# Kernel optimization log

Hardware: AMD Instinct MI355X
Metric: run time of the kernel (lower is better)

## Reference

```python
import jax, jax.numpy as jnp
import numpy as np

N = 1_000_000   # pose-graph nodes
E = 2_000_000   # edges (odometry + loop closures)
M = N - 1
L1, L2, L3, L4 = 1.0, 0.1, 1.0, 0.1  # loss weights
EPS = 1e-8

# ---- quaternion / Lie-group helpers (pypose convention: [x,y,z,w]) ----

def qmul(q, r):
    qv, qw = q[..., :3], q[..., 3:]
    rv, rw = r[..., :3], r[..., 3:]
    w = qw * rw - jnp.sum(qv * rv, axis=-1, keepdims=True)
    v = qw * rv + rw * qv + jnp.cross(qv, rv)
    return jnp.concatenate([v, w], axis=-1)

def qconj(q):  # inverse of a unit quaternion
    return jnp.concatenate([-q[..., :3], q[..., 3:]], axis=-1)

def qrot(q, v):  # rotate vector v by unit quaternion q
    qv, qw = q[..., :3], q[..., 3:]
    t = 2.0 * jnp.cross(qv, v)
    return v + qw * t + jnp.cross(qv, t)

def so3_log(q):  # SO3 -> so3 rotation vector phi
    v, w = q[..., :3], q[..., 3]
    n = jnp.linalg.norm(v, axis=-1)
    theta = 2.0 * jnp.arctan2(n, w)
    big = n > EPS
    k = jnp.where(big, theta / jnp.where(big, n, 1.0), 2.0 / jnp.where(jnp.abs(w) > EPS, w, 1.0))
    return v * k[..., None]

def se3_log(t, q):  # SE3 -> se3 = [tau(3), phi(3)] (translation first, pypose order)
    phi = so3_log(q)
    theta2 = jnp.sum(phi * phi, axis=-1)
    theta = jnp.sqrt(theta2)
    small = theta < 1e-4
    ts = jnp.where(small, 1.0, theta)
    # V^{-1} coefficient: 1/theta^2 - (1+cos)/(2 theta sin); Taylor -> 1/12
    coef = jnp.where(small, 1.0 / 12.0,
                     1.0 / jnp.where(small, 1.0, theta2)
                     - (1.0 + jnp.cos(ts)) / (2.0 * ts * jnp.sin(ts)))
    pxt = jnp.cross(phi, t)
    tau = t - 0.5 * pxt + coef[..., None] * jnp.cross(phi, pxt)  # V^{-1} t without 3x3 mats
    return jnp.concatenate([tau, phi], axis=-1)

def _unit_quat(key, n):
    q = jax.random.normal(key, (n, 4), dtype=jnp.float32)
    return q / jnp.linalg.norm(q, axis=-1, keepdims=True)

def setup_inputs() -> dict:
    key = jax.random.key(0)
    k = jax.random.split(key, 9)
    nodes = jnp.concatenate([jax.random.normal(k[0], (N, 3), jnp.float32), _unit_quat(k[1], N)], axis=-1)
    vels = jax.random.normal(k[2], (N, 3), jnp.float32)
    edges = jax.random.randint(k[3], (E, 2), 0, N, dtype=jnp.int32)
    poses = jnp.concatenate([jax.random.normal(k[4], (E, 3), jnp.float32), _unit_quat(k[5], E)], axis=-1)
    imu_drots = _unit_quat(k[6], M)
    imu_dtrans = 0.1 * jax.random.normal(k[7], (M, 3), jnp.float32)
    imu_dvels = 0.1 * jax.random.normal(k[8], (M, 3), jnp.float32)
    dts = jnp.full((M, 1), 0.05, dtype=jnp.float32)
    return dict(edges=edges, nodes=nodes, vels=vels, poses=poses,
                imu_drots=imu_drots, imu_dtrans=imu_dtrans, imu_dvels=imu_dvels, dts=dts)

def reference(edges, nodes, vels, poses, imu_drots, imu_dtrans, imu_dvels, dts):
    t_n, q_n = nodes[:, :3], nodes[:, 3:]
    # --- pose-graph residual: (poses^-1 o node1^-1 o node2).Log() ---
    n1 = nodes[edges[:, 0]]
    n2 = nodes[edges[:, 1]]
    t1, q1 = n1[:, :3], n1[:, 3:]
    t2, q2 = n2[:, :3], n2[:, 3:]
    tp, qp = poses[:, :3], poses[:, 3:]
    qi1 = qconj(q1)
    ti1 = -qrot(qi1, t1)           # node1^-1
    qa = qmul(qi1, q2)
    ta = ti1 + qrot(qi1, t2)       # node1^-1 o node2
    qip = qconj(qp)
    tip = -qrot(qip, tp)           # poses^-1
    qe = qmul(qip, qa)
    te = tip + qrot(qip, ta)
    pgerr = se3_log(te, qe)                                   # [E, 6]
    # --- adjacent velocity residual ---
    adjvelerr = imu_dvels - (vels[1:] - vels[:-1])            # [M, 3]
    # --- IMU rotation residual: (drot^-1 o R1^-1 o R2).Log() ---
    qre = qmul(qconj(imu_drots), qmul(qconj(q_n[:-1]), q_n[1:]))
    imuroterr = so3_log(qre)                                  # [M, 3]
    # --- translation/velocity residual ---
    transvelerr = (t_n[1:] - t_n[:-1]) - (vels[:-1] * dts + imu_dtrans)  # [M, 3]
    return jnp.concatenate([L1 * pgerr.ravel(), L2 * adjvelerr.ravel(),
                            L3 * imuroterr.ravel(), L4 * transvelerr.ravel()], axis=0)
```

## Files before the change

kernel.cpp:

```cpp
#include <hip/hip_runtime.h>
#include <math.h>

#define EPS_Q 1e-8f

struct F3 { float x, y, z; };
struct Q4 { F3 v; float w; };

__device__ __forceinline__ F3 add3(F3 a, F3 b){ return {a.x+b.x, a.y+b.y, a.z+b.z}; }
__device__ __forceinline__ F3 sub3(F3 a, F3 b){ return {a.x-b.x, a.y-b.y, a.z-b.z}; }
__device__ __forceinline__ F3 scal3(float s, F3 a){ return {s*a.x, s*a.y, s*a.z}; }
__device__ __forceinline__ float dot3(F3 a, F3 b){ return a.x*b.x + a.y*b.y + a.z*b.z; }
__device__ __forceinline__ F3 cross3(F3 a, F3 b){
    return { a.y*b.z - a.z*b.y, a.z*b.x - a.x*b.z, a.x*b.y - a.y*b.x };
}

__device__ __forceinline__ Q4 qmul(Q4 q, Q4 r){
    Q4 o;
    o.w = q.w*r.w - dot3(q.v, r.v);
    o.v = add3(add3(scal3(q.w, r.v), scal3(r.w, q.v)), cross3(q.v, r.v));
    return o;
}
__device__ __forceinline__ Q4 qconj(Q4 q){ return { {-q.v.x, -q.v.y, -q.v.z}, q.w }; }
__device__ __forceinline__ F3 qrot(Q4 q, F3 v){
    F3 t = scal3(2.0f, cross3(q.v, v));
    return add3(add3(v, scal3(q.w, t)), cross3(q.v, t));
}
__device__ __forceinline__ F3 so3_log(Q4 q){
    float n = sqrtf(dot3(q.v, q.v));
    float theta = 2.0f * atan2f(n, q.w);
    float k;
    if (n > EPS_Q) k = theta / n;
    else           k = 2.0f / ((fabsf(q.w) > EPS_Q) ? q.w : 1.0f);
    return scal3(k, q.v);
}

__global__ void edge_kernel(const int*   __restrict__ edges,
                            const float* __restrict__ nodes,
                            const float* __restrict__ poses,
                            float*       __restrict__ out,
                            int E)
{
    int e = blockIdx.x * blockDim.x + threadIdx.x;
    if (e >= E) return;

    int i = edges[2*(size_t)e];
    int j = edges[2*(size_t)e + 1];
    const float* n1 = nodes + 7*(size_t)i;
    const float* n2 = nodes + 7*(size_t)j;
    const float* p  = poses + 7*(size_t)e;

    F3 t1 = {n1[0], n1[1], n1[2]};  Q4 q1 = {{n1[3], n1[4], n1[5]}, n1[6]};
    F3 t2 = {n2[0], n2[1], n2[2]};  Q4 q2 = {{n2[3], n2[4], n2[5]}, n2[6]};
    F3 tp = {p[0],  p[1],  p[2]};   Q4 qp = {{p[3],  p[4],  p[5]},  p[6]};

    Q4 qi1 = qconj(q1);
    F3 ti1 = scal3(-1.0f, qrot(qi1, t1));
    Q4 qa  = qmul(qi1, q2);
    F3 ta  = add3(ti1, qrot(qi1, t2));

    Q4 qip = qconj(qp);
    F3 tip = scal3(-1.0f, qrot(qip, tp));
    Q4 qe  = qmul(qip, qa);
    F3 te  = add3(tip, qrot(qip, ta));

    F3 phi = so3_log(qe);
    float theta2 = dot3(phi, phi);
    float theta  = sqrtf(theta2);
    float coef;
    if (theta < 1e-4f) {
        coef = 1.0f / 12.0f;
    } else {
        coef = 1.0f / theta2 - (1.0f + cosf(theta)) / (2.0f * theta * sinf(theta));
    }
    F3 pxt = cross3(phi, te);
    F3 tau = add3(sub3(te, scal3(0.5f, pxt)), scal3(coef, cross3(phi, pxt)));

    float* o = out + 6*(size_t)e;
    o[0] = tau.x; o[1] = tau.y; o[2] = tau.z;
    o[3] = phi.x; o[4] = phi.y; o[5] = phi.z;
}

__global__ void node_kernel(const float* __restrict__ nodes,
                            const float* __restrict__ vels,
                            const float* __restrict__ imu_drots,
                            const float* __restrict__ imu_dtrans,
                            const float* __restrict__ imu_dvels,
                            const float* __restrict__ dts,
                            float*       __restrict__ out,
                            int M,
                            size_t off_adjvel, size_t off_imurot, size_t off_transvel)
{
    int m = blockIdx.x * blockDim.x + threadIdx.x;
    if (m >= M) return;

    const float* n0 = nodes + 7*(size_t)m;
    const float* n1 = nodes + 7*(size_t)(m+1);
    F3 t0 = {n0[0], n0[1], n0[2]};  Q4 q0 = {{n0[3], n0[4], n0[5]}, n0[6]};
    F3 t1 = {n1[0], n1[1], n1[2]};  Q4 q1 = {{n1[3], n1[4], n1[5]}, n1[6]};

    F3 v0 = {vels[3*(size_t)m],     vels[3*(size_t)m + 1], vels[3*(size_t)m + 2]};
    F3 v1 = {vels[3*(size_t)m + 3], vels[3*(size_t)m + 4], vels[3*(size_t)m + 5]};

    F3 dvm = {imu_dvels[3*(size_t)m], imu_dvels[3*(size_t)m + 1], imu_dvels[3*(size_t)m + 2]};
    F3 adjv = sub3(dvm, sub3(v1, v0));
    out[off_adjvel + 3*(size_t)m    ] = 0.1f * adjv.x;
    out[off_adjvel + 3*(size_t)m + 1] = 0.1f * adjv.y;
    out[off_adjvel + 3*(size_t)m + 2] = 0.1f * adjv.z;

    Q4 dr = {{imu_drots[4*(size_t)m], imu_drots[4*(size_t)m + 1], imu_drots[4*(size_t)m + 2]},
              imu_drots[4*(size_t)m + 3]};
    Q4 qre = qmul(qconj(dr), qmul(qconj(q0), q1));
    F3 rot = so3_log(qre);
    out[off_imurot + 3*(size_t)m    ] = rot.x;
    out[off_imurot + 3*(size_t)m + 1] = rot.y;
    out[off_imurot + 3*(size_t)m + 2] = rot.z;

    float dt = dts[m];
    F3 dtr = {imu_dtrans[3*(size_t)m], imu_dtrans[3*(size_t)m + 1], imu_dtrans[3*(size_t)m + 2]};
    F3 tv = sub3(sub3(t1, t0), add3(scal3(dt, v0), dtr));
    out[off_transvel + 3*(size_t)m    ] = 0.1f * tv.x;
    out[off_transvel + 3*(size_t)m + 1] = 0.1f * tv.y;
    out[off_transvel + 3*(size_t)m + 2] = 0.1f * tv.z;
}

extern "C" void kernel_launch(void* const* d_in, const int* in_sizes, int n_in,
                              void* d_out, int out_size, void* d_ws, size_t ws_size,
                              hipStream_t stream) {
    const int*   edges      = (const int*)  d_in[0];
    const float* nodes      = (const float*)d_in[1];
    const float* vels       = (const float*)d_in[2];
    const float* poses      = (const float*)d_in[3];
    const float* imu_drots  = (const float*)d_in[4];
    const float* imu_dtrans = (const float*)d_in[5];
    const float* imu_dvels  = (const float*)d_in[6];
    const float* dts        = (const float*)d_in[7];
    float* out = (float*)d_out;

    const int E = in_sizes[0] / 2;
    const int M = in_sizes[7];

    const size_t off_adjvel   = 6*(size_t)E;
    const size_t off_imurot   = off_adjvel + 3*(size_t)M;
    const size_t off_transvel = off_imurot + 3*(size_t)M;

    const int BLK = 256;
    edge_kernel<<<(E + BLK - 1) / BLK, BLK, 0, stream>>>(edges, nodes, poses, out, E);
    node_kernel<<<(M + BLK - 1) / BLK, BLK, 0, stream>>>(nodes, vels, imu_drots, imu_dtrans,
                                                         imu_dvels, dts, out, M,
                                                         off_adjvel, off_imurot, off_transvel);
}
```

Baseline: 271.8 us.

## Fuse edge and node kernels into one interleaved launch with nontemporal streaming

Merges the edge residual kernel and the node residual kernel into a single launch. Node blocks are spread evenly among edge blocks through a proportional block-index mapping, so both workloads run concurrently instead of one after the other. Streaming inputs and all outputs use nontemporal loads and stores so that the randomly gathered node table stays in cache, the IMU quaternion is read as one vector load, and sincosf replaces separate sin and cos calls. Block-to-work mapping becomes more complex, and the nontemporal hints could hurt if the hardware handles them poorly.

Measured after the change: 275.9 us. No clear change (+1.5%).

```diff
diff --git a/kernel.cpp b/kernel.cpp
--- a/kernel.cpp
+++ b/kernel.cpp
@@ -5,6 +5,8 @@
 
 struct F3 { float x, y, z; };
 struct Q4 { F3 v; float w; };
+
+typedef float fvec4 __attribute__((ext_vector_type(4)));
 
 __device__ __forceinline__ F3 add3(F3 a, F3 b){ return {a.x+b.x, a.y+b.y, a.z+b.z}; }
 __device__ __forceinline__ F3 sub3(F3 a, F3 b){ return {a.x-b.x, a.y-b.y, a.z-b.z}; }
@@ -34,93 +36,109 @@
     return scal3(k, q.v);
 }
 
-__global__ void edge_kernel(const int*   __restrict__ edges,
-                            const float* __restrict__ nodes,
-                            const float* __restrict__ poses,
-                            float*       __restrict__ out,
-                            int E)
+__device__ __forceinline__ float ntl (const float* p){ return __builtin_nontemporal_load(p); }
+__device__ __forceinline__ int   ntli(const int*   p){ return __builtin_nontemporal_load(p); }
+__device__ __forceinline__ void  nts (float* p, float v){ __builtin_nontemporal_store(v, p); }
+
+__global__ __launch_bounds__(256)
+void fused_kernel(const int*   __restrict__ edges,
+                  const float* __restrict__ nodes,
+                  const float* __restrict__ vels,
+                  const float* __restrict__ poses,
+                  const float* __restrict__ imu_drots,
+                  const float* __restrict__ imu_dtrans,
+                  const float* __restrict__ imu_dvels,
+                  const float* __restrict__ dts,
+                  float*       __restrict__ out,
+                  int E, int M, int NB, int T,
+                  size_t off_adjvel, size_t off_imurot, size_t off_transvel)
 {
-    int e = blockIdx.x * blockDim.x + threadIdx.x;
-    if (e >= E) return;
+    const int b   = blockIdx.x;
+    const int tid = threadIdx.x;
+    const long long f0 = ((long long)b       * NB) / T;
+    const long long f1 = ((long long)(b + 1) * NB) / T;
 
-    int i = edges[2*(size_t)e];
-    int j = edges[2*(size_t)e + 1];
-    const float* n1 = nodes + 7*(size_t)i;
-    const float* n2 = nodes + 7*(size_t)j;
-    const float* p  = poses + 7*(size_t)e;
+    if (f1 > f0) {
+        const int m = (int)f0 * 256 + tid;
+        if (m >= M) return;
 
-    F3 t1 = {n1[0], n1[1], n1[2]};  Q4 q1 = {{n1[3], n1[4], n1[5]}, n1[6]};
-    F3 t2 = {n2[0], n2[1], n2[2]};  Q4 q2 = {{n2[3], n2[4], n2[5]}, n2[6]};
-    F3 tp = {p[0],  p[1],  p[2]};   Q4 qp = {{p[3],  p[4],  p[5]},  p[6]};
+        const float* n0  = nodes + 7*(size_t)m;
+        const float* n1p = nodes + 7*(size_t)(m+1);
+        F3 t0 = {n0[0],  n0[1],  n0[2]};   Q4 q0 = {{n0[3],  n0[4],  n0[5]},  n0[6]};
+        F3 t1 = {n1p[0], n1p[1], n1p[2]};  Q4 q1 = {{n1p[3], n1p[4], n1p[5]}, n1p[6]};
 
-    Q4 qi1 = qconj(q1);
-    F3 ti1 = scal3(-1.0f, qrot(qi1, t1));
-    Q4 qa  = qmul(qi1, q2);
-    F3 ta  = add3(ti1, qrot(qi1, t2));
+        F3 v0 = {vels[3*(size_t)m],     vels[3*(size_t)m + 1], vels[3*(size_t)m + 2]};
+        F3 v1 = {vels[3*(size_t)m + 3], vels[3*(size_t)m + 4], vels[3*(size_t)m + 5]};
 
-    Q4 qip = qconj(qp);
-    F3 tip = scal3(-1.0f, qrot(qip, tp));
-    Q4 qe  = qmul(qip, qa);
-    F3 te  = add3(tip, qrot(qip, ta));
+        fvec4 drq = __builtin_nontemporal_load(reinterpret_cast<const fvec4*>(imu_drots) + m);
+        Q4 dr = {{drq.x, drq.y, drq.z}, drq.w};
 
-    F3 phi = so3_log(qe);
-    float theta2 = dot3(phi, phi);
-    float theta  = sqrtf(theta2);
-    float coef;
-    if (theta < 1e-4f) {
-        coef = 1.0f / 12.0f;
+        F3 dvm = { ntl(imu_dvels + 3*(size_t)m),
+                   ntl(imu_dvels + 3*(size_t)m + 1),
+                   ntl(imu_dvels + 3*(size_t)m + 2) };
+        F3 dtr = { ntl(imu_dtrans + 3*(size_t)m),
+                   ntl(imu_dtrans + 3*(size_t)m + 1),
+                   ntl(imu_dtrans + 3*(size_t)m + 2) };
+        float dt = ntl(dts + m);
+
+        F3 adjv = sub3(dvm, sub3(v1, v0));
+        nts(out + off_adjvel + 3*(size_t)m,     0.1f * adjv.x);
+        nts(out + off_adjvel + 3*(size_t)m + 1, 0.1f * adjv.y);
+        nts(out + off_adjvel + 3*(size_t)m + 2, 0.1f * adjv.z);
+
+        Q4 qre = qmul(qconj(dr), qmul(qconj(q0), q1));
+        F3 rot = so3_log(qre);
+        nts(out + off_imurot + 3*(size_t)m,     rot.x);
+        nts(out + off_imurot + 3*(size_t)m + 1, rot.y);
+        nts(out + off_imurot + 3*(size_t)m + 2, rot.z);
+
+        F3 tv = sub3(sub3(t1, t0), add3(scal3(dt, v0), dtr));
+        nts(out + off_transvel + 3*(size_t)m,     0.1f * tv.x);
+        nts(out + off_transvel + 3*(size_t)m + 1, 0.1f * tv.y);
+        nts(out + off_transvel + 3*(size_t)m + 2, 0.1f * tv.z);
     } else {
-        coef = 1.0f / theta2 - (1.0f + cosf(theta)) / (2.0f * theta * sinf(theta));
+        const int e = (b - (int)f0) * 256 + tid;
+        if (e >= E) return;
+
+        int i = ntli(edges + 2*(size_t)e);
+        int j = ntli(edges + 2*(size_t)e + 1);
+        const float* n1 = nodes + 7*(size_t)i;
+        const float* n2 = nodes + 7*(size_t)j;
+        const float* p  = poses + 7*(size_t)e;
+
+        F3 t1 = {n1[0], n1[1], n1[2]};  Q4 q1 = {{n1[3], n1[4], n1[5]}, n1[6]};
+        F3 t2 = {n2[0], n2[1], n2[2]};  Q4 q2 = {{n2[3], n2[4], n2[5]}, n2[6]};
+        F3 tp = {ntl(p+0), ntl(p+1), ntl(p+2)};
+        Q4 qp = {{ntl(p+3), ntl(p+4), ntl(p+5)}, ntl(p+6)};
+
+        Q4 qi1 = qconj(q1);
+        F3 ti1 = scal3(-1.0f, qrot(qi1, t1));
+        Q4 qa  = qmul(qi1, q2);
+        F3 ta  = add3(ti1, qrot(qi1, t2));
+
+        Q4 qip = qconj(qp);
+        F3 tip = scal3(-1.0f, qrot(qip, tp));
+        Q4 qe  = qmul(qip, qa);
+        F3 te  = add3(tip, qrot(qip, ta));
+
+        F3 phi = so3_log(qe);
+        float theta2 = dot3(phi, phi);
+        float theta  = sqrtf(theta2);
+        float coef;
+        if (theta < 1e-4f) {
+            coef = 1.0f / 12.0f;
+        } else {
+            float s, c;
+            sincosf(theta, &s, &c);
+            coef = 1.0f / theta2 - (1.0f + c) / (2.0f * theta * s);
+        }
+        F3 pxt = cross3(phi, te);
+        F3 tau = add3(sub3(te, scal3(0.5f, pxt)), scal3(coef, cross3(phi, pxt)));
+
+        float* o = out + 6*(size_t)e;
+        nts(o,   tau.x); nts(o+1, tau.y); nts(o+2, tau.z);
+        nts(o+3, phi.x); nts(o+4, phi.y); nts(o+5, phi.z);
     }
-    F3 pxt = cross3(phi, te);
-    F3 tau = add3(sub3(te, scal3(0.5f, pxt)), scal3(coef, cross3(phi, pxt)));
-
-    float* o = out + 6*(size_t)e;
-    o[0] = tau.x; o[1] = tau.y; o[2] = tau.z;
-    o[3] = phi.x; o[4] = phi.y; o[5] = phi.z;
-}
-
-__global__ void node_kernel(const float* __restrict__ nodes,
-                            const float* __restrict__ vels,
-                            const float* __restrict__ imu_drots,
-                            const float* __restrict__ imu_dtrans,
-                            const float* __restrict__ imu_dvels,
-                            const float* __restrict__ dts,
-                            float*       __restrict__ out,
-                            int M,
-                            size_t off_adjvel, size_t off_imurot, size_t off_transvel)
-{
-    int m = blockIdx.x * blockDim.x + threadIdx.x;
-    if (m >= M) return;
-
-    const float* n0 = nodes + 7*(size_t)m;
-    const float* n1 = nodes + 7*(size_t)(m+1);
-    F3 t0 = {n0[0], n0[1], n0[2]};  Q4 q0 = {{n0[3], n0[4], n0[5]}, n0[6]};
-    F3 t1 = {n1[0], n1[1], n1[2]};  Q4 q1 = {{n1[3], n1[4], n1[5]}, n1[6]};
-
-    F3 v0 = {vels[3*(size_t)m],     vels[3*(size_t)m + 1], vels[3*(size_t)m + 2]};
-    F3 v1 = {vels[3*(size_t)m + 3], vels[3*(size_t)m + 4], vels[3*(size_t)m + 5]};
-
-    F3 dvm = {imu_dvels[3*(size_t)m], imu_dvels[3*(size_t)m + 1], imu_dvels[3*(size_t)m + 2]};
-    F3 adjv = sub3(dvm, sub3(v1, v0));
-    out[off_adjvel + 3*(size_t)m    ] = 0.1f * adjv.x;
-    out[off_adjvel + 3*(size_t)m + 1] = 0.1f * adjv.y;
-    out[off_adjvel + 3*(size_t)m + 2] = 0.1f * adjv.z;
-
-    Q4 dr = {{imu_drots[4*(size_t)m], imu_drots[4*(size_t)m + 1], imu_drots[4*(size_t)m + 2]},
-              imu_drots[4*(size_t)m + 3]};
-    Q4 qre = qmul(qconj(dr), qmul(qconj(q0), q1));
-    F3 rot = so3_log(qre);
-    out[off_imurot + 3*(size_t)m    ] = rot.x;
-    out[off_imurot + 3*(size_t)m + 1] = rot.y;
-    out[off_imurot + 3*(size_t)m + 2] = rot.z;
-
-    float dt = dts[m];
-    F3 dtr = {imu_dtrans[3*(size_t)m], imu_dtrans[3*(size_t)m + 1], imu_dtrans[3*(size_t)m + 2]};
-    F3 tv = sub3(sub3(t1, t0), add3(scal3(dt, v0), dtr));
-    out[off_transvel + 3*(size_t)m    ] = 0.1f * tv.x;
-    out[off_transvel + 3*(size_t)m + 1] = 0.1f * tv.y;
-    out[off_transvel + 3*(size_t)m + 2] = 0.1f * tv.z;
 }
 
 extern "C" void kernel_launch(void* const* d_in, const int* in_sizes, int n_in,
@@ -144,8 +162,12 @@
     const size_t off_transvel = off_imurot + 3*(size_t)M;
 
     const int BLK = 256;
-    edge_kernel<<<(E + BLK - 1) / BLK, BLK, 0, stream>>>(edges, nodes, poses, out, E);
-    node_kernel<<<(M + BLK - 1) / BLK, BLK, 0, stream>>>(nodes, vels, imu_drots, imu_dtrans,
-                                                         imu_dvels, dts, out, M,
-                                                         off_adjvel, off_imurot, off_transvel);
+    const int EB = (E + BLK - 1) / BLK;
+    const int NB = (M + BLK - 1) / BLK;
+    const int T  = EB + NB;
+
+    fused_kernel<<<T, BLK, 0, stream>>>(edges, nodes, vels, poses,
+                                        imu_drots, imu_dtrans, imu_dvels, dts,
+                                        out, E, M, NB, T,
+                                        off_adjvel, off_imurot, off_transvel);
 }
```
